# Kernel tuning notes

Measured on AMD Instinct MI355X. Metric: run time of the kernel, lower is better.

## Reference

```python
import jax, jax.numpy as jnp
import numpy as np

N, L, H, D, F, C = 2048, 2, 4, 16, 64, 32
E = H * D  # 64
EPS = 1e-5


def _layernorm(x, gamma, beta):
    # LayerNorm over last dim (size D)
    mu = jnp.mean(x, axis=-1, keepdims=True)
    var = jnp.mean((x - mu) ** 2, axis=-1, keepdims=True)
    return (x - mu) * jax.lax.rsqrt(var + EPS) * gamma + beta


def _nodewise_ffn(feat, w0, b0, w1, b1, gamma, beta):
    # feat: (N,L,E); w0: (N,L,H,F,E); w1: (N,L,H,F,D)
    h = jnp.einsum('nle,nlhfe->nlhf', feat, w0) + b0
    h = jax.nn.relu(h)                                   # dropout = identity (eval)
    out = jnp.einsum('nlhf,nlhfd->nlhd', h, w1) + b1     # (N,L,H,D)
    return _layernorm(out, gamma, beta)


def setup_inputs() -> dict:
    key = jax.random.key(0)
    ks = jax.random.split(key, 12)
    s_w = 0.05  # keep per-node FFN outputs in a sane range
    return {
        'feat': jax.random.normal(ks[0], (N, L, E), jnp.float32),
        'query': jax.random.normal(ks[1], (N, L, H, D), jnp.float32),
        'kw0': jax.random.normal(ks[2], (N, L, H, F, E), jnp.float32) * s_w,
        'kb0': jax.random.normal(ks[3], (N, L, H, F), jnp.float32) * s_w,
        'kw1': jax.random.normal(ks[4], (N, L, H, F, D), jnp.float32) * s_w,
        'kb1': jax.random.normal(ks[5], (N, L, H, D), jnp.float32) * s_w,
        'vw0': jax.random.normal(ks[6], (N, L, H, F, E), jnp.float32) * s_w,
        'vb0': jax.random.normal(ks[7], (N, L, H, F), jnp.float32) * s_w,
        'vw1': jax.random.normal(ks[8], (N, L, H, F, D), jnp.float32) * s_w,
        'vb1': jax.random.normal(ks[9], (N, L, H, D), jnp.float32) * s_w,
        'key_gamma': jnp.ones((D,), jnp.float32),
        'key_beta': jnp.zeros((D,), jnp.float32),
        'out_gamma': jnp.ones((D,), jnp.float32),
        'out_beta': jnp.zeros((D,), jnp.float32),
        'component_id': jax.random.randint(ks[10], (N,), 0, C).astype(jnp.int64),
    }


def reference(feat, query, kw0, kb0, kw1, kb1, vw0, vb0, vw1, vb1,
              key_gamma, key_beta, out_gamma, out_beta, component_id):
    # NOTE: original module (faithfully) reuses key_norm for the value path.
    key_t = _nodewise_ffn(feat, kw0, kb0, kw1, kb1, key_gamma, key_beta)   # (N,L,H,D)
    value = _nodewise_ffn(feat, vw0, vb0, vw1, vb1, key_gamma, key_beta)   # (N,L,H,D)

    unique_component_id = jnp.unique(component_id)                          # (C,)
    logits = jnp.sum(key_t * query, axis=-1)                                # (N,L,H)

    # component-masked softmax over (node, layer) jointly, per (component, head)
    comp_mask = unique_component_id[:, None] != component_id[None, :]       # (C,N)
    masked = jnp.where(comp_mask[:, :, None, None], -1e9, logits[None])     # (C,N,L,H)
    Cn = masked.shape[0]
    attn = jax.nn.softmax(masked.reshape(Cn, N * L, H), axis=1)
    attn = attn.reshape(Cn, N, L, H)                                        # (C,N,L,H)

    out = jnp.einsum('cnlh,nlhd->chd', attn, value)                         # (C,H,D)
    out = _layernorm(out, out_gamma, out_beta)
    return out.reshape(Cn, H * D), attn, unique_component_id
```

## Files before the change

### kernel.cpp

```cpp
#include <hip/hip_runtime.h>
#include <cstdint>
#include <cstddef>

#define NN 2048
#define LL 2
#define HH 4
#define DD 16
#define FF 64
#define CC 32
#define EE 64
#define ML (NN*LL)

__global__ __launch_bounds__(256) void k_unique(const int* __restrict__ comp,
                                                int* __restrict__ presence,
                                                int* __restrict__ unique_out,
                                                float* __restrict__ uniq_f_out)
{
    int t = threadIdx.x;
    if (t < 64) presence[t] = 0;
    __syncthreads();
    for (int n = t; n < NN; n += 256) {
        int v = comp[n];
        if (v >= 0 && v < 64) presence[v] = 1;
    }
    __syncthreads();
    if (t < 64) {
        int rank = 0;
        for (int u = 0; u < t; ++u) rank += presence[u];
        if (presence[t]) {
            unique_out[rank] = t;
            uniq_f_out[rank] = (float)t;
        }
    }
}

__global__ __launch_bounds__(512) void k_ffn(
    const float* __restrict__ feat, const float* __restrict__ query,
    const float* __restrict__ kw0, const float* __restrict__ kb0,
    const float* __restrict__ kw1, const float* __restrict__ kb1,
    const float* __restrict__ vw0, const float* __restrict__ vb0,
    const float* __restrict__ vw1, const float* __restrict__ vb1,
    const float* __restrict__ gamma, const float* __restrict__ beta,
    float* __restrict__ ws_logits, float* __restrict__ ws_value)
{
    const int m = blockIdx.x;
    const int t = threadIdx.x;
    const int w = t >> 6;
    const int L = t & 63;
    const int p = w >> 2;
    const int h = w & 3;

    __shared__ float h_lds[8][64];

    const size_t mh = (size_t)(m * HH + h);
    const float* w0 = (p ? vw0 : kw0) + mh * (FF * EE);
    const float* b0 = (p ? vb0 : kb0) + mh * FF;
    const float* w1 = (p ? vw1 : kw1) + mh * (FF * DD);
    const float* b1 = (p ? vb1 : kb1) + mh * DD;

    float4 f4 = *(const float4*)(feat + (size_t)m * EE + 4 * (L & 15));

    #pragma unroll
    for (int it = 0; it < 16; ++it) {
        float4 wv = *(const float4*)(w0 + it * 256 + 4 * L);
        float s = wv.x * f4.x + wv.y * f4.y + wv.z * f4.z + wv.w * f4.w;
        s += __shfl_xor(s, 1, 64);
        s += __shfl_xor(s, 2, 64);
        s += __shfl_xor(s, 4, 64);
        s += __shfl_xor(s, 8, 64);
        if ((L & 15) == 0) h_lds[w][it * 4 + (L >> 4)] = s;
    }
    __syncthreads();

    float4 acc = make_float4(0.f, 0.f, 0.f, 0.f);
    #pragma unroll
    for (int i = 0; i < 4; ++i) {
        float4 wv = *(const float4*)(w1 + i * 256 + 4 * L);
        int f = i * 16 + (L >> 2);
        float hv = h_lds[w][f] + b0[f];
        hv = hv > 0.f ? hv : 0.f;
        acc.x += hv * wv.x; acc.y += hv * wv.y;
        acc.z += hv * wv.z; acc.w += hv * wv.w;
    }
    #pragma unroll
    for (int mask = 4; mask <= 32; mask <<= 1) {
        acc.x += __shfl_xor(acc.x, mask, 64);
        acc.y += __shfl_xor(acc.y, mask, 64);
        acc.z += __shfl_xor(acc.z, mask, 64);
        acc.w += __shfl_xor(acc.w, mask, 64);
    }
    const int dg = L & 3;
    float4 bv = *(const float4*)(b1 + 4 * dg);
    acc.x += bv.x; acc.y += bv.y; acc.z += bv.z; acc.w += bv.w;

    float s = acc.x + acc.y + acc.z + acc.w;
    s += __shfl_xor(s, 1, 64);
    s += __shfl_xor(s, 2, 64);
    float mu = s * (1.f / 16.f);
    float d0 = acc.x - mu, d1 = acc.y - mu, d2 = acc.z - mu, d3 = acc.w - mu;
    float q = d0 * d0 + d1 * d1 + d2 * d2 + d3 * d3;
    q += __shfl_xor(q, 1, 64);
    q += __shfl_xor(q, 2, 64);
    float rstd = rsqrtf(q * (1.f / 16.f) + 1e-5f);
    float4 gv = *(const float4*)(gamma + 4 * dg);
    float4 be = *(const float4*)(beta + 4 * dg);
    float4 y;
    y.x = d0 * rstd * gv.x + be.x;
    y.y = d1 * rstd * gv.y + be.y;
    y.z = d2 * rstd * gv.z + be.z;
    y.w = d3 * rstd * gv.w + be.w;

    if (p == 0) {
        float4 qv = *(const float4*)(query + mh * DD + 4 * dg);
        float lg = y.x * qv.x + y.y * qv.y + y.z * qv.z + y.w * qv.w;
        lg += __shfl_xor(lg, 1, 64);
        lg += __shfl_xor(lg, 2, 64);
        if (L == 0) ws_logits[m * HH + h] = lg;
    } else {
        if (L < 4) *(float4*)(ws_value + mh * DD + 4 * L) = y;
    }
}

__global__ __launch_bounds__(256) void k_softmax_out(
    const float* __restrict__ logits, const float* __restrict__ value,
    const int* __restrict__ comp, const int* __restrict__ unique,
    const float* __restrict__ out_gamma, const float* __restrict__ out_beta,
    float* __restrict__ out0, float* __restrict__ attn_out)
{
    const int c = blockIdx.x;
    const int t = threadIdx.x;
    const int h = t & 3;
    const int g = t >> 2;
    const int uc = unique[c];

    __shared__ float red[HH][64];
    __shared__ float accs[256][16];

    float mx = -3.0e38f;
    for (int k = 0; k < 64; ++k) {
        int m = g + (k << 6);
        int n = m >> 1;
        float lv = logits[m * HH + h];
        float x = (comp[n] == uc) ? lv : -1e9f;
        mx = fmaxf(mx, x);
    }
    red[h][g] = mx;
    __syncthreads();
    for (int s = 32; s >= 1; s >>= 1) {
        if (g < s) red[h][g] = fmaxf(red[h][g], red[h][g + s]);
        __syncthreads();
    }
    const float maxv = red[h][0];
    __syncthreads();

    float se = 0.f;
    for (int k = 0; k < 64; ++k) {
        int m = g + (k << 6);
        int n = m >> 1;
        float lv = logits[m * HH + h];
        float x = (comp[n] == uc) ? lv : -1e9f;
        se += expf(x - maxv);
    }
    red[h][g] = se;
    __syncthreads();
    for (int s = 32; s >= 1; s >>= 1) {
        if (g < s) red[h][g] += red[h][g + s];
        __syncthreads();
    }
    const float inv = 1.f / red[h][0];

    float4 a0 = make_float4(0.f,0.f,0.f,0.f), a1 = a0, a2 = a0, a3 = a0;
    for (int k = 0; k < 64; ++k) {
        int m = g + (k << 6);
        int n = m >> 1;
        bool mem = (comp[n] == uc);
        float lv = logits[m * HH + h];
        float x = mem ? lv : -1e9f;
        float at = expf(x - maxv) * inv;
        attn_out[(size_t)c * (ML * HH) + m * HH + h] = at;
        if (mem) {
            const float4* vp = (const float4*)(value + (size_t)(m * HH + h) * DD);
            float4 v0 = vp[0], v1 = vp[1], v2 = vp[2], v3 = vp[3];
            a0.x += at*v0.x; a0.y += at*v0.y; a0.z += at*v0.z; a0.w += at*v0.w;
            a1.x += at*v1.x; a1.y += at*v1.y; a1.z += at*v1.z; a1.w += at*v1.w;
            a2.x += at*v2.x; a2.y += at*v2.y; a2.z += at*v2.z; a2.w += at*v2.w;
            a3.x += at*v3.x; a3.y += at*v3.y; a3.z += at*v3.z; a3.w += at*v3.w;
        }
    }
    accs[t][0]=a0.x;  accs[t][1]=a0.y;  accs[t][2]=a0.z;  accs[t][3]=a0.w;
    accs[t][4]=a1.x;  accs[t][5]=a1.y;  accs[t][6]=a1.z;  accs[t][7]=a1.w;
    accs[t][8]=a2.x;  accs[t][9]=a2.y;  accs[t][10]=a2.z; accs[t][11]=a2.w;
    accs[t][12]=a3.x; accs[t][13]=a3.y; accs[t][14]=a3.z; accs[t][15]=a3.w;
    __syncthreads();
    for (int s = 32; s >= 1; s >>= 1) {
        if (g < s) {
            #pragma unroll
            for (int j = 0; j < 16; ++j) accs[t][j] += accs[t + 4 * s][j];
        }
        __syncthreads();
    }

    if (t < 64) {
        int hh = t >> 4, d = t & 15;
        float val = accs[hh][d];
        float s = val;
        s += __shfl_xor(s, 1, 64); s += __shfl_xor(s, 2, 64);
        s += __shfl_xor(s, 4, 64); s += __shfl_xor(s, 8, 64);
        float mu = s * (1.f / 16.f);
        float dx = val - mu;
        float q = dx * dx;
        q += __shfl_xor(q, 1, 64); q += __shfl_xor(q, 2, 64);
        q += __shfl_xor(q, 4, 64); q += __shfl_xor(q, 8, 64);
        float rstd = rsqrtf(q * (1.f / 16.f) + 1e-5f);
        out0[c * 64 + t] = dx * rstd * out_gamma[d] + out_beta[d];
    }
}

extern "C" void kernel_launch(void* const* d_in, const int* in_sizes, int n_in,
                              void* d_out, int out_size, void* d_ws, size_t ws_size,
                              hipStream_t stream) {
    const float* feat      = (const float*)d_in[0];
    const float* query     = (const float*)d_in[1];
    const float* kw0       = (const float*)d_in[2];
    const float* kb0       = (const float*)d_in[3];
    const float* kw1       = (const float*)d_in[4];
    const float* kb1       = (const float*)d_in[5];
    const float* vw0       = (const float*)d_in[6];
    const float* vb0       = (const float*)d_in[7];
    const float* vw1       = (const float*)d_in[8];
    const float* vb1       = (const float*)d_in[9];
    const float* key_gamma = (const float*)d_in[10];
    const float* key_beta  = (const float*)d_in[11];
    const float* out_gamma = (const float*)d_in[12];
    const float* out_beta  = (const float*)d_in[13];
    const int*   comp      = (const int*)d_in[14];

    float* out = (float*)d_out;
    float* out0     = out;
    float* attn_out = out + CC * 64;
    float* uniq_f   = out + CC * 64 + (size_t)CC * ML * HH;

    float* wsf       = (float*)d_ws;
    float* ws_logits = wsf;
    float* ws_value  = wsf + ML * HH;
    int*   ws_pres   = (int*)(wsf + ML * HH + (size_t)ML * HH * DD);
    int*   ws_unique = ws_pres + 64;

    hipLaunchKernelGGL(k_unique, dim3(1), dim3(256), 0, stream,
                       comp, ws_pres, ws_unique, uniq_f);
    hipLaunchKernelGGL(k_ffn, dim3(ML), dim3(512), 0, stream,
                       feat, query, kw0, kb0, kw1, kb1, vw0, vb0, vw1, vb1,
                       key_gamma, key_beta, ws_logits, ws_value);
    hipLaunchKernelGGL(k_softmax_out, dim3(CC), dim3(256), 0, stream,
                       ws_logits, ws_value, comp, ws_unique,
                       out_gamma, out_beta, out0, attn_out);
}
```

Before: 647.5 us.

## Split softmax-aggregate across heads and precompute node component ranks

The softmax/aggregation kernel now runs on a grid of components by heads, so four times as many blocks run. Each thread keeps its 16 logits in registers across the max, sum and weighted-value passes instead of re-reading them three times. Logits are stored transposed per head for coalesced loads, and k_unique precomputes a per-node component rank so membership is one integer compare. The shared-memory tree reductions become wave shuffles, at the cost of more registers per thread and strided attn writes.

```diff
diff --git a/kernel.cpp b/kernel.cpp
--- a/kernel.cpp
+++ b/kernel.cpp
@@ -12,25 +12,34 @@
 #define ML (NN*LL)
 
 __global__ __launch_bounds__(256) void k_unique(const int* __restrict__ comp,
-                                                int* __restrict__ presence,
+                                                int* __restrict__ rank_out,
                                                 int* __restrict__ unique_out,
+                                                int* __restrict__ count_out,
                                                 float* __restrict__ uniq_f_out)
 {
+    __shared__ int pres[64];
+    __shared__ int rankOf[64];
     int t = threadIdx.x;
-    if (t < 64) presence[t] = 0;
+    if (t < 64) pres[t] = 0;
     __syncthreads();
     for (int n = t; n < NN; n += 256) {
         int v = comp[n];
-        if (v >= 0 && v < 64) presence[v] = 1;
+        if (v >= 0 && v < 64) pres[v] = 1;
     }
     __syncthreads();
     if (t < 64) {
         int rank = 0;
-        for (int u = 0; u < t; ++u) rank += presence[u];
-        if (presence[t]) {
+        for (int u = 0; u < t; ++u) rank += pres[u];
+        rankOf[t] = rank;
+        if (pres[t]) {
             unique_out[rank] = t;
             uniq_f_out[rank] = (float)t;
         }
+        if (t == 63) count_out[0] = rank + pres[63];
+    }
+    __syncthreads();
+    for (int n = t; n < NN; n += 256) {
+        rank_out[n] = rankOf[comp[n] & 63];
     }
 }
 
@@ -41,7 +50,7 @@
     const float* __restrict__ vw0, const float* __restrict__ vb0,
     const float* __restrict__ vw1, const float* __restrict__ vb1,
     const float* __restrict__ gamma, const float* __restrict__ beta,
-    float* __restrict__ ws_logits, float* __restrict__ ws_value)
+    float* __restrict__ ws_logitsT, float* __restrict__ ws_value)
 {
     const int m = blockIdx.x;
     const int t = threadIdx.x;
@@ -115,94 +124,90 @@
         float lg = y.x * qv.x + y.y * qv.y + y.z * qv.z + y.w * qv.w;
         lg += __shfl_xor(lg, 1, 64);
         lg += __shfl_xor(lg, 2, 64);
-        if (L == 0) ws_logits[m * HH + h] = lg;
+        if (L == 0) ws_logitsT[h * ML + m] = lg;
     } else {
         if (L < 4) *(float4*)(ws_value + mh * DD + 4 * L) = y;
     }
 }
 
 __global__ __launch_bounds__(256) void k_softmax_out(
-    const float* __restrict__ logits, const float* __restrict__ value,
-    const int* __restrict__ comp, const int* __restrict__ unique,
+    const float* __restrict__ logitsT, const float* __restrict__ value,
+    const int* __restrict__ rank, const int* __restrict__ count,
     const float* __restrict__ out_gamma, const float* __restrict__ out_beta,
     float* __restrict__ out0, float* __restrict__ attn_out)
 {
     const int c = blockIdx.x;
+    const int h = blockIdx.y;
     const int t = threadIdx.x;
-    const int h = t & 3;
-    const int g = t >> 2;
-    const int uc = unique[c];
-
-    __shared__ float red[HH][64];
-    __shared__ float accs[256][16];
-
-    float mx = -3.0e38f;
-    for (int k = 0; k < 64; ++k) {
-        int m = g + (k << 6);
-        int n = m >> 1;
-        float lv = logits[m * HH + h];
-        float x = (comp[n] == uc) ? lv : -1e9f;
-        mx = fmaxf(mx, x);
-    }
-    red[h][g] = mx;
-    __syncthreads();
-    for (int s = 32; s >= 1; s >>= 1) {
-        if (g < s) red[h][g] = fmaxf(red[h][g], red[h][g + s]);
-        __syncthreads();
-    }
-    const float maxv = red[h][0];
+    const int w = t >> 6;
+    const int L = t & 63;
+    if (c >= count[0]) return;
+
+    __shared__ float red[4];
+    __shared__ float wacc[4][16];
+
+    float x[16];
+    bool mem[16];
+    #pragma unroll
+    for (int i = 0; i < 16; ++i) {
+        int m = t + i * 256;
+        float lv = logitsT[h * ML + m];
+        mem[i] = (rank[m >> 1] == c);
+        x[i] = mem[i] ? lv : -1e9f;
+    }
+
+    float mx = x[0];
+    #pragma unroll
+    for (int i = 1; i < 16; ++i) mx = fmaxf(mx, x[i]);
+    #pragma unroll
+    for (int msk = 1; msk <= 32; msk <<= 1) mx = fmaxf(mx, __shfl_xor(mx, msk, 64));
+    if (L == 0) red[w] = mx;
+    __syncthreads();
+    mx = fmaxf(fmaxf(red[0], red[1]), fmaxf(red[2], red[3]));
     __syncthreads();
 
     float se = 0.f;
-    for (int k = 0; k < 64; ++k) {
-        int m = g + (k << 6);
-        int n = m >> 1;
-        float lv = logits[m * HH + h];
-        float x = (comp[n] == uc) ? lv : -1e9f;
-        se += expf(x - maxv);
-    }
-    red[h][g] = se;
-    __syncthreads();
-    for (int s = 32; s >= 1; s >>= 1) {
-        if (g < s) red[h][g] += red[h][g + s];
-        __syncthreads();
-    }
-    const float inv = 1.f / red[h][0];
-
-    float4 a0 = make_float4(0.f,0.f,0.f,0.f), a1 = a0, a2 = a0, a3 = a0;
-    for (int k = 0; k < 64; ++k) {
-        int m = g + (k << 6);
-        int n = m >> 1;
-        bool mem = (comp[n] == uc);
-        float lv = logits[m * HH + h];
-        float x = mem ? lv : -1e9f;
-        float at = expf(x - maxv) * inv;
-        attn_out[(size_t)c * (ML * HH) + m * HH + h] = at;
-        if (mem) {
+    #pragma unroll
+    for (int i = 0; i < 16; ++i) {
+        x[i] = __expf(x[i] - mx) == 0.f ? expf(x[i] - mx) : expf(x[i] - mx);
+        se += x[i];
+    }
+    #pragma unroll
+    for (int msk = 1; msk <= 32; msk <<= 1) se += __shfl_xor(se, msk, 64);
+    if (L == 0) red[w] = se;
+    __syncthreads();
+    const float inv = 1.f / (red[0] + red[1] + red[2] + red[3]);
+
+    float acc[16];
+    #pragma unroll
+    for (int j = 0; j < 16; ++j) acc[j] = 0.f;
+    #pragma unroll
+    for (int i = 0; i < 16; ++i) {
+        int m = t + i * 256;
+        float at = x[i] * inv;
+        attn_out[(size_t)c * (ML * HH) + (size_t)m * HH + h] = at;
+        if (mem[i]) {
             const float4* vp = (const float4*)(value + (size_t)(m * HH + h) * DD);
             float4 v0 = vp[0], v1 = vp[1], v2 = vp[2], v3 = vp[3];
-            a0.x += at*v0.x; a0.y += at*v0.y; a0.z += at*v0.z; a0.w += at*v0.w;
-            a1.x += at*v1.x; a1.y += at*v1.y; a1.z += at*v1.z; a1.w += at*v1.w;
-            a2.x += at*v2.x; a2.y += at*v2.y; a2.z += at*v2.z; a2.w += at*v2.w;
-            a3.x += at*v3.x; a3.y += at*v3.y; a3.z += at*v3.z; a3.w += at*v3.w;
+            acc[0]+=at*v0.x; acc[1]+=at*v0.y; acc[2]+=at*v0.z; acc[3]+=at*v0.w;
+            acc[4]+=at*v1.x; acc[5]+=at*v1.y; acc[6]+=at*v1.z; acc[7]+=at*v1.w;
+            acc[8]+=at*v2.x; acc[9]+=at*v2.y; acc[10]+=at*v2.z; acc[11]+=at*v2.w;
+            acc[12]+=at*v3.x; acc[13]+=at*v3.y; acc[14]+=at*v3.z; acc[15]+=at*v3.w;
         }
     }
-    accs[t][0]=a0.x;  accs[t][1]=a0.y;  accs[t][2]=a0.z;  accs[t][3]=a0.w;
-    accs[t][4]=a1.x;  accs[t][5]=a1.y;  accs[t][6]=a1.z;  accs[t][7]=a1.w;
-    accs[t][8]=a2.x;  accs[t][9]=a2.y;  accs[t][10]=a2.z; accs[t][11]=a2.w;
-    accs[t][12]=a3.x; accs[t][13]=a3.y; accs[t][14]=a3.z; accs[t][15]=a3.w;
-    __syncthreads();
-    for (int s = 32; s >= 1; s >>= 1) {
-        if (g < s) {
-            #pragma unroll
-            for (int j = 0; j < 16; ++j) accs[t][j] += accs[t + 4 * s][j];
-        }
-        __syncthreads();
-    }
-
-    if (t < 64) {
-        int hh = t >> 4, d = t & 15;
-        float val = accs[hh][d];
+    #pragma unroll
+    for (int j = 0; j < 16; ++j) {
+        #pragma unroll
+        for (int msk = 1; msk <= 32; msk <<= 1) acc[j] += __shfl_xor(acc[j], msk, 64);
+    }
+    if (L == 0) {
+        #pragma unroll
+        for (int j = 0; j < 16; ++j) wacc[w][j] = acc[j];
+    }
+    __syncthreads();
+
+    if (t < 16) {
+        float val = wacc[0][t] + wacc[1][t] + wacc[2][t] + wacc[3][t];
         float s = val;
         s += __shfl_xor(s, 1, 64); s += __shfl_xor(s, 2, 64);
         s += __shfl_xor(s, 4, 64); s += __shfl_xor(s, 8, 64);
@@ -212,7 +217,7 @@
         q += __shfl_xor(q, 1, 64); q += __shfl_xor(q, 2, 64);
         q += __shfl_xor(q, 4, 64); q += __shfl_xor(q, 8, 64);
         float rstd = rsqrtf(q * (1.f / 16.f) + 1e-5f);
-        out0[c * 64 + t] = dx * rstd * out_gamma[d] + out_beta[d];
+        out0[c * 64 + h * 16 + t] = dx * rstd * out_gamma[t] + out_beta[t];
     }
 }
 
@@ -240,18 +245,19 @@
     float* attn_out = out + CC * 64;
     float* uniq_f   = out + CC * 64 + (size_t)CC * ML * HH;
 
-    float* wsf       = (float*)d_ws;
-    float* ws_logits = wsf;
-    float* ws_value  = wsf + ML * HH;
-    int*   ws_pres   = (int*)(wsf + ML * HH + (size_t)ML * HH * DD);
-    int*   ws_unique = ws_pres + 64;
+    float* wsf        = (float*)d_ws;
+    float* ws_logitsT = wsf;
+    float* ws_value   = wsf + HH * ML;
+    int*   ws_rank    = (int*)(wsf + HH * ML + (size_t)ML * HH * DD);
+    int*   ws_unique  = ws_rank + NN;
+    int*   ws_count   = ws_unique + 64;
 
     hipLaunchKernelGGL(k_unique, dim3(1), dim3(256), 0, stream,
-                       comp, ws_pres, ws_unique, uniq_f);
+                       comp, ws_rank, ws_unique, ws_count, uniq_f);
     hipLaunchKernelGGL(k_ffn, dim3(ML), dim3(512), 0, stream,
                        feat, query, kw0, kb0, kw1, kb1, vw0, vb0, vw1, vb1,
-                       key_gamma, key_beta, ws_logits, ws_value);
-    hipLaunchKernelGGL(k_softmax_out, dim3(CC), dim3(256), 0, stream,
-                       ws_logits, ws_value, comp, ws_unique,
+                       key_gamma, key_beta, ws_logitsT, ws_value);
+    hipLaunchKernelGGL(k_softmax_out, dim3(CC, HH), dim3(256), 0, stream,
+                       ws_logitsT, ws_value, ws_rank, ws_count,
                        out_gamma, out_beta, out0, attn_out);
 }
```

Measured after the change: 610.8 us. 5.7% less time.
